# Kernel optimization log

Hardware: AMD Instinct MI355X
Metric: run time of the kernel (lower is better)

## Reference

```python
import jax, jax.numpy as jnp
import numpy as np

B, S, H, A, F = 16, 512, 768, 12, 3072
DH = H // A  # 64
EPS = 1e-5

def layernorm(x, w, b):
    mu = jnp.mean(x, axis=-1, keepdims=True)
    var = jnp.mean(jnp.square(x - mu), axis=-1, keepdims=True)
    return (x - mu) * jax.lax.rsqrt(var + EPS) * w + b

def setup_inputs() -> dict:
    key = jax.random.key(0)
    ks = jax.random.split(key, 12)
    std = 0.02
    inp = {
        "X": jax.random.normal(ks[0], (B, S, H), jnp.float32),
        "mask": jax.random.randint(ks[1], (B, S), 0, 2, jnp.int32),
        "WQ": jax.random.normal(ks[2], (H, H), jnp.float32) * std,
        "bQ": jnp.zeros((H,), jnp.float32),
        "WK": jax.random.normal(ks[3], (H, H), jnp.float32) * std,
        "bK": jnp.zeros((H,), jnp.float32),
        "WV": jax.random.normal(ks[4], (H, H), jnp.float32) * std,
        "bV": jnp.zeros((H,), jnp.float32),
        "WO": jax.random.normal(ks[5], (H, H), jnp.float32) * std,
        "bO": jnp.zeros((H,), jnp.float32),
        "ln1_w": jnp.ones((H,), jnp.float32),
        "ln1_b": jnp.zeros((H,), jnp.float32),
        "W1": jax.random.normal(ks[6], (H, F), jnp.float32) * std,
        "b1": jnp.zeros((F,), jnp.float32),
        "W2": jax.random.normal(ks[7], (F, H), jnp.float32) * std,
        "b2": jnp.zeros((H,), jnp.float32),
        "ln2_w": jnp.ones((H,), jnp.float32),
        "ln2_b": jnp.zeros((H,), jnp.float32),
    }
    return inp

def reference(X, mask, WQ, bQ, WK, bK, WV, bV, WO, bO, ln1_w, ln1_b, W1, b1, W2, b2, ln2_w, ln2_b):
    # --- multi-head self-attention (pretrained-weights branch, faithful reshapes) ---
    Q = (X @ WQ + bQ).reshape(B, A, S, DH)
    K = (X @ WK + bK).reshape(B, A, S, DH)
    V = (X @ WV + bV).reshape(B, A, S, DH)
    scores = jnp.einsum('bhqd,bhkd->bhqk', Q, K) / jnp.sqrt(jnp.float32(DH))
    scores = jnp.where(mask[:, None, None, :] == 0, -jnp.inf, scores)
    attn = jax.nn.softmax(scores, axis=-1)
    Z = jnp.einsum('bhqk,bhkd->bhqd', attn, V).reshape(B, S, H)
    attn_out = Z @ WO + bO
    # residual + LN (dropout is identity in eval)
    X = layernorm(attn_out + X, ln1_w, ln1_b)
    # --- FFN with exact GELU ---
    ffn = jax.nn.gelu(X @ W1 + b1, approximate=False) @ W2 + b2
    X = layernorm(ffn + X, ln2_w, ln2_b)
    return X
```

## Files before the change

kernel.cpp:

```cpp
#include <hip/hip_runtime.h>
#include <hip/hip_bf16.h>


using bf16_t = __hip_bfloat16;
typedef __bf16 bf16x8 __attribute__((ext_vector_type(8)));
typedef float f32x4 __attribute__((ext_vector_type(4)));

__device__ __forceinline__ float b2f(bf16_t v) { return __bfloat162float(v); }
__device__ __forceinline__ bf16_t f2b(float v) { return __float2bfloat16(v); }
__device__ __forceinline__ ushort f2bu(float v) { bf16_t b = f2b(v); return *(ushort*)&b; }

__device__ __forceinline__ void glds16(const ushort* g, ushort* l) {
    __builtin_amdgcn_global_load_lds(
        (const __attribute__((address_space(1))) unsigned int*)g,
        (__attribute__((address_space(3))) unsigned int*)l, 16, 0, 0);
}

__device__ __forceinline__ float gelu_f(float x) {
    float x2 = x * x;
    float y2 = 1.5957691216057308f * x * fmaf(0.044715f, x2, 1.0f);
    float e = __expf(y2);
    float t = 1.f - 2.f / (e + 1.f);
    return 0.5f * x * (1.f + t);
}

__device__ __forceinline__ void tr_tile(const float* __restrict__ in,
                                        bf16_t* __restrict__ out,
                                        int R, int C, int tx, int ty,
                                        float (*t)[65], int tid)
{
    int r0 = ty * 64, c0 = tx * 64;
    int tr = tid >> 6, tc = tid & 63;
#pragma unroll 4
    for (int i = 0; i < 16; ++i) {
        int r = i * 4 + tr;
        t[r][tc] = in[(size_t)(r0 + r) * C + c0 + tc];
    }
    __syncthreads();
#pragma unroll 4
    for (int i = 0; i < 16; ++i) {
        int r = i * 4 + tr;
        out[(size_t)(c0 + r) * R + r0 + tc] = f2b(t[tc][r]);
    }
}

__global__ __launch_bounds__(256) void prep_kernel(
    const float* __restrict__ WQ, const float* __restrict__ WK,
    const float* __restrict__ WV, const float* __restrict__ WO,
    const float* __restrict__ W1, const float* __restrict__ W2,
    const float* __restrict__ bQ, const float* __restrict__ bK,
    const float* __restrict__ bV, const float* __restrict__ X,
    bf16_t* __restrict__ Wqkv, bf16_t* __restrict__ WOt,
    bf16_t* __restrict__ W1t, bf16_t* __restrict__ W2t,
    float* __restrict__ bcat, bf16_t* __restrict__ Xb)
{
    __shared__ float t[64][65];
    const int blk = blockIdx.x, tid = threadIdx.x;
    if (blk < 576) {
        int m = blk / 144, tt = blk % 144;
        const float* in = (m == 0) ? WQ : (m == 1) ? WK : (m == 2) ? WV : WO;
        bf16_t* out = (m == 0) ? Wqkv : (m == 1) ? Wqkv + 589824
                    : (m == 2) ? Wqkv + 1179648 : WOt;
        tr_tile(in, out, 768, 768, tt % 12, tt / 12, t, tid);
    } else if (blk < 1152) {
        int tt = blk - 576;
        tr_tile(W1, W1t, 768, 3072, tt % 48, tt / 48, t, tid);
    } else if (blk < 1728) {
        int tt = blk - 1152;
        tr_tile(W2, W2t, 3072, 768, tt % 12, tt / 12, t, tid);
    } else if (blk == 1728) {
        for (int i = tid; i < 2304; i += 256)
            bcat[i] = (i < 768) ? bQ[i] : (i < 1536) ? bK[i - 768] : bV[i - 1536];
    } else {
        size_t i = ((size_t)(blk - 1729) * 256 + tid) * 8;
        float4 a = *(const float4*)(X + i);
        float4 b = *(const float4*)(X + i + 4);
#pragma unroll
        for (int j = 0; j < 4; ++j) {
            Xb[i + j]     = f2b(((const float*)&a)[j]);
            Xb[i + 4 + j] = f2b(((const float*)&b)[j]);
        }
    }
}

__global__ __launch_bounds__(256) void transpose_bf(
    const ushort* __restrict__ in, ushort* __restrict__ out,
    int R, int C, long inB, long outB)
{
    __shared__ ushort t[64][65];
    const ushort* ip = in + (size_t)blockIdx.z * inB;
    ushort* op = out + (size_t)blockIdx.z * outB;
    int r0 = blockIdx.y * 64, c0 = blockIdx.x * 64;
    int tr = threadIdx.x >> 6, tc = threadIdx.x & 63;
#pragma unroll 4
    for (int i = 0; i < 16; ++i) {
        int r = i * 4 + tr;
        t[r][tc] = ip[(size_t)(r0 + r) * C + c0 + tc];
    }
    __syncthreads();
#pragma unroll 4
    for (int i = 0; i < 16; ++i) {
        int r = i * 4 + tr;
        op[(size_t)(c0 + r) * R + r0 + tc] = t[tc][r];
    }
}

template <int EPI, int NTILE>
__global__ __launch_bounds__(256) void gemm128(
    const bf16_t* __restrict__ A, const bf16_t* __restrict__ Bt,
    const float* __restrict__ bias, const void* __restrict__ res,
    void* __restrict__ Cv, int K, int lda, int ldb, int ldc)
{
    __shared__ ushort lA[128 * 64];
    __shared__ ushort lB[NTILE * 64];
    constexpr int NI = NTILE / 32;
    const int tid = threadIdx.x;
    const int l = tid & 63, w = tid >> 6;
    const int l16 = l & 15, quad = l >> 4;
    const int m0 = blockIdx.x * 128, n0 = blockIdx.y * NTILE;

    const int srow = tid >> 3;
    const int sg = (((tid & 7) ^ (srow & 7)) << 3);
    const ushort* gA = (const ushort*)A + (size_t)(m0 + srow) * lda + sg;
    const ushort* gB = (const ushort*)Bt + (size_t)(n0 + srow) * ldb + sg;
    ushort* dA = lA + tid * 8;
    ushort* dB = lB + tid * 8;

    f32x4 acc[4][NI] = {};
    const int arow = (w & 1) * 64;
    const int brow = (w >> 1) * (NTILE / 2);

    for (int k0 = 0; k0 < K; k0 += 64) {
        __syncthreads();
        glds16(gA + k0,                      dA);
        glds16(gA + k0 + (size_t)32 * lda,   dA + 2048);
        glds16(gA + k0 + (size_t)64 * lda,   dA + 4096);
        glds16(gA + k0 + (size_t)96 * lda,   dA + 6144);
        glds16(gB + k0,                      dB);
        glds16(gB + k0 + (size_t)32 * ldb,   dB + 2048);
        if constexpr (NTILE == 128) {
            glds16(gB + k0 + (size_t)64 * ldb, dB + 4096);
            glds16(gB + k0 + (size_t)96 * ldb, dB + 6144);
        }
        __syncthreads();
#pragma unroll
        for (int kk = 0; kk < 2; ++kk) {
            const int pc = (((kk * 4 + quad) ^ (l16 & 7)) << 3);
            bf16x8 bfr[NI];
#pragma unroll
            for (int ni = 0; ni < NI; ++ni)
                bfr[ni] = *(const bf16x8*)&lB[(brow + ni * 16 + l16) * 64 + pc];
#pragma unroll
            for (int mi = 0; mi < 4; ++mi) {
                bf16x8 afr = *(const bf16x8*)&lA[(arow + mi * 16 + l16) * 64 + pc];
#pragma unroll
                for (int ni = 0; ni < NI; ++ni)
                    acc[mi][ni] = __builtin_amdgcn_mfma_f32_16x16x32_bf16(bfr[ni], afr, acc[mi][ni], 0, 0, 0);
            }
        }
    }

    float4 bv4[NI];
#pragma unroll
    for (int ni = 0; ni < NI; ++ni)
        bv4[ni] = *(const float4*)&bias[n0 + brow + ni * 16 + quad * 4];

#pragma unroll
    for (int mi = 0; mi < 4; ++mi) {
        int m = m0 + arow + mi * 16 + l16;
#pragma unroll
        for (int ni = 0; ni < NI; ++ni) {
            int nb = n0 + brow + ni * 16 + quad * 4;
            float v[4];
#pragma unroll
            for (int r = 0; r < 4; ++r) v[r] = acc[mi][ni][r] + ((const float*)&bv4[ni])[r];
            if constexpr (EPI == 1) {
#pragma unroll
                for (int r = 0; r < 4; ++r) v[r] = gelu_f(v[r]);
            } else if constexpr (EPI == 2) {
                float4 r4 = *(const float4*)&((const float*)res)[(size_t)m * ldc + nb];
#pragma unroll
                for (int r = 0; r < 4; ++r) v[r] += ((const float*)&r4)[r];
            } else if constexpr (EPI == 5) {
                ushort4 rb = *(const ushort4*)&((const ushort*)res)[(size_t)m * ldc + nb];
#pragma unroll
                for (int r = 0; r < 4; ++r) v[r] += b2f(*(const bf16_t*)&((const ushort*)&rb)[r]);
            }
            if constexpr (EPI == 5) {
                *(float4*)&((float*)Cv)[(size_t)m * ldc + nb] = make_float4(v[0], v[1], v[2], v[3]);
            } else {
                ushort4 st;
                st.x = f2bu(v[0]); st.y = f2bu(v[1]); st.z = f2bu(v[2]); st.w = f2bu(v[3]);
                if constexpr (EPI == 6) {
                    bf16_t* Cseg = (bf16_t*)Cv + (size_t)(n0 / 768) * 6291456;
                    int nloc = (n0 % 768) + brow + ni * 16 + quad * 4;
                    *(ushort4*)&((ushort*)Cseg)[(size_t)m * 768 + nloc] = st;
                } else {
                    *(ushort4*)&((ushort*)Cv)[(size_t)m * ldc + nb] = st;
                }
            }
        }
    }
}

__global__ __launch_bounds__(256) void flash_kernel(
    const bf16_t* __restrict__ Q, const bf16_t* __restrict__ Kx,
    const bf16_t* __restrict__ Vt, const int* __restrict__ mask,
    bf16_t* __restrict__ Z)
{
    __shared__ ushort lK[64 * 64];
    __shared__ ushort lV[64 * 64];
    __shared__ ushort lP[64 * 72];

    const int h = blockIdx.y;
    const int q0 = blockIdx.x * 64;
    const ushort* Qh = (const ushort*)Q + (size_t)h * 32768;
    const ushort* Kh = (const ushort*)Kx + (size_t)h * 32768;
    const ushort* Vh = (const ushort*)Vt + (size_t)h * 32768;
    const int* mk = mask + (h / 12) * 512;
    ushort* Zh = (ushort*)Z + (size_t)h * 32768;

    const int tid = threadIdx.x;
    const int l = tid & 63, w = tid >> 6;
    const int l16 = l & 15, quad = l >> 4;

    bf16x8 qfr[2];
#pragma unroll
    for (int kk = 0; kk < 2; ++kk)
        qfr[kk] = *(const bf16x8*)(Qh + (size_t)(q0 + w * 16 + l16) * 64 + kk * 32 + quad * 8);

    const int c8p = tid & 7;
    const int kr0 = tid >> 3;
    float m_i = -1e30f, l_i = 0.f;
    f32x4 o4[4] = {};

    for (int kt = 0; kt < 8; ++kt) {
#pragma unroll
        for (int p = 0; p < 2; ++p) {
            int row = kr0 + p * 32;
            int c8l = c8p ^ (row & 7);
            glds16(Kh + (size_t)(kt * 64 + row) * 64 + c8l * 8, lK + (p * 256 + tid) * 8);
            glds16(Vh + (size_t)row * 512 + kt * 64 + c8l * 8, lV + (p * 256 + tid) * 8);
        }
        __syncthreads();

        f32x4 s4[4] = {};
#pragma unroll
        for (int kk = 0; kk < 2; ++kk) {
#pragma unroll
            for (int nt = 0; nt < 4; ++nt) {
                bf16x8 kfr = *(const bf16x8*)&lK[(nt * 16 + l16) * 64 + (((kk * 4 + quad) ^ (l16 & 7)) << 3)];
                s4[nt] = __builtin_amdgcn_mfma_f32_16x16x32_bf16(kfr, qfr[kk], s4[nt], 0, 0, 0);
            }
        }

        float pv[4][4];
        float rm = -1e30f;
#pragma unroll
        for (int nt = 0; nt < 4; ++nt) {
            int4 m4 = *(const int4*)&mk[kt * 64 + nt * 16 + quad * 4];
#pragma unroll
            for (int r = 0; r < 4; ++r) {
                float v = (((const int*)&m4)[r] == 0) ? -1e30f : s4[nt][r] * 0.125f;
                pv[nt][r] = v;
                rm = fmaxf(rm, v);
            }
        }
        rm = fmaxf(rm, __shfl_xor(rm, 16));
        rm = fmaxf(rm, __shfl_xor(rm, 32));
        float mn = fmaxf(m_i, rm);
        float al = __expf(m_i - mn);
        float rs = 0.f;
#pragma unroll
        for (int nt = 0; nt < 4; ++nt)
#pragma unroll
            for (int r = 0; r < 4; ++r) {
                float e = __expf(pv[nt][r] - mn);
                pv[nt][r] = e;
                rs += e;
            }
        rs += __shfl_xor(rs, 16);
        rs += __shfl_xor(rs, 32);
        l_i = l_i * al + rs;
        m_i = mn;
#pragma unroll
        for (int dt = 0; dt < 4; ++dt)
#pragma unroll
            for (int r = 0; r < 4; ++r) o4[dt][r] *= al;

#pragma unroll
        for (int nt = 0; nt < 4; ++nt) {
            ushort4 st;
            st.x = f2bu(pv[nt][0]); st.y = f2bu(pv[nt][1]);
            st.z = f2bu(pv[nt][2]); st.w = f2bu(pv[nt][3]);
            *(ushort4*)&lP[(w * 16 + l16) * 72 + nt * 16 + quad * 4] = st;
        }
        __syncthreads();

#pragma unroll
        for (int kk = 0; kk < 2; ++kk) {
            bf16x8 pafr = *(const bf16x8*)&lP[(w * 16 + l16) * 72 + kk * 32 + quad * 8];
#pragma unroll
            for (int dt = 0; dt < 4; ++dt) {
                bf16x8 bvfr = *(const bf16x8*)&lV[(dt * 16 + l16) * 64 + (((kk * 4 + quad) ^ (l16 & 7)) << 3)];
                o4[dt] = __builtin_amdgcn_mfma_f32_16x16x32_bf16(bvfr, pafr, o4[dt], 0, 0, 0);
            }
        }
        __syncthreads();
    }

    float inv = 1.f / l_i;
#pragma unroll
    for (int dt = 0; dt < 4; ++dt) {
        ushort4 st;
        st.x = f2bu(o4[dt][0] * inv); st.y = f2bu(o4[dt][1] * inv);
        st.z = f2bu(o4[dt][2] * inv); st.w = f2bu(o4[dt][3] * inv);
        *(ushort4*)&Zh[(size_t)(q0 + w * 16 + l16) * 64 + dt * 16 + quad * 4] = st;
    }
}

__device__ __forceinline__ float to_f(float v)  { return v; }
__device__ __forceinline__ float to_f(bf16_t v) { return b2f(v); }
__device__ __forceinline__ void from_f(float& d, float v)  { d = v; }
__device__ __forceinline__ void from_f(bf16_t& d, float v) { d = f2b(v); }

template <typename TI, typename TO>
__global__ __launch_bounds__(256) void layernorm_kernel(
    const TI* __restrict__ X, const float* __restrict__ w,
    const float* __restrict__ b, TO* __restrict__ out)
{
    const TI* x = X + (size_t)blockIdx.x * 768;
    TO* o = out + (size_t)blockIdx.x * 768;
    int t = threadIdx.x;
    float v[3];
    float s = 0.f, sq = 0.f;
#pragma unroll
    for (int i = 0; i < 3; ++i) {
        v[i] = to_f(x[t + i * 256]);
        s += v[i]; sq += v[i] * v[i];
    }
#pragma unroll
    for (int off = 32; off; off >>= 1) { s += __shfl_xor(s, off); sq += __shfl_xor(sq, off); }
    __shared__ float s1[4], s2[4];
    int wave = t >> 6, lane = t & 63;
    if (lane == 0) { s1[wave] = s; s2[wave] = sq; }
    __syncthreads();
    s  = s1[0] + s1[1] + s1[2] + s1[3];
    sq = s2[0] + s2[1] + s2[2] + s2[3];
    float mu  = s * (1.f / 768.f);
    float var = sq * (1.f / 768.f) - mu * mu;
    float rs  = rsqrtf(var + 1e-5f);
#pragma unroll
    for (int i = 0; i < 3; ++i)
        from_f(o[t + i * 256], (v[i] - mu) * rs * w[t + i * 256] + b[t + i * 256]);
}

extern "C" void kernel_launch(void* const* d_in, const int* in_sizes, int n_in,
                              void* d_out, int out_size, void* d_ws, size_t ws_size,
                              hipStream_t stream)
{
    const float* X    = (const float*)d_in[0];
    const int*   mask = (const int*)  d_in[1];
    const float* WQ   = (const float*)d_in[2];
    const float* bQ   = (const float*)d_in[3];
    const float* WK   = (const float*)d_in[4];
    const float* bK   = (const float*)d_in[5];
    const float* WV   = (const float*)d_in[6];
    const float* bV   = (const float*)d_in[7];
    const float* WO   = (const float*)d_in[8];
    const float* bO   = (const float*)d_in[9];
    const float* ln1w = (const float*)d_in[10];
    const float* ln1b = (const float*)d_in[11];
    const float* W1   = (const float*)d_in[12];
    const float* b1   = (const float*)d_in[13];
    const float* W2   = (const float*)d_in[14];
    const float* b2   = (const float*)d_in[15];
    const float* ln2w = (const float*)d_in[16];
    const float* ln2b = (const float*)d_in[17];
    float* out = (float*)d_out;

    bf16_t* ws   = (bf16_t*)d_ws;
    bf16_t* Wqkv = ws;
    bf16_t* WOt  = Wqkv + 1769472;
    bf16_t* W1t  = WOt + 589824;
    bf16_t* W2t  = W1t + 2359296;
    float*  bcat = (float*)(W2t + 2359296);
    bf16_t* Qb   = W2t + 2359296 + 4608;
    bf16_t* Kb   = Qb + 6291456;
    bf16_t* Vb   = Kb + 6291456;
    bf16_t* Xb   = Vb + 6291456;
    bf16_t* Vt   = Xb + 6291456;
    bf16_t* Zb = Qb;
    bf16_t* Y1 = Xb;
    bf16_t* X1 = Qb;
    bf16_t* Hb = Kb;

    prep_kernel<<<4801, 256, 0, stream>>>(WQ, WK, WV, WO, W1, W2, bQ, bK, bV, X,
                                          Wqkv, WOt, W1t, W2t, bcat, Xb);

    gemm128<6, 128><<<dim3(64, 18), 256, 0, stream>>>(Xb, Wqkv, bcat, nullptr, Qb,
                                                      768, 768, 768, 768);

    transpose_bf<<<dim3(1, 8, 192), 256, 0, stream>>>((const ushort*)Vb, (ushort*)Vt,
                                                      512, 64, 32768, 32768);

    flash_kernel<<<dim3(8, 192), 256, 0, stream>>>(Qb, Kb, Vt, mask, Zb);

    gemm128<2, 64><<<dim3(64, 12), 256, 0, stream>>>(Zb, WOt, bO, X, Y1,
                                                     768, 768, 768, 768);
    layernorm_kernel<bf16_t, bf16_t><<<8192, 256, 0, stream>>>(Y1, ln1w, ln1b, X1);

    gemm128<1, 128><<<dim3(64, 24), 256, 0, stream>>>(X1, W1t, b1, nullptr, Hb,
                                                      768, 768, 768, 3072);
    gemm128<5, 64><<<dim3(64, 12), 256, 0, stream>>>(Hb, W2t, b2, X1, out,
                                                     3072, 3072, 3072, 768);
    layernorm_kernel<float, float><<<8192, 256, 0, stream>>>(out, ln2w, ln2b, out);
}
```

Baseline: 379.7 us.

## Fuse V transpose into QKV GEMM epilogue and double flash query tile

The QKV GEMM epilogue now writes the V segment straight into the per-head transposed layout, which removes the separate transpose kernel launch and one round trip of V through memory. The flash attention kernel now handles 128 query rows per block, two 16-row MFMA subtiles per wave, so each K/V tile loaded into LDS is reused twice as much. The cost is scattered 2-byte strided stores in the GEMM epilogue, more registers and LDS in the flash kernel, and half as many flash blocks.

```diff
diff --git a/kernel.cpp b/kernel.cpp
--- a/kernel.cpp
+++ b/kernel.cpp
@@ -83,28 +83,6 @@
     }
 }
 
-__global__ __launch_bounds__(256) void transpose_bf(
-    const ushort* __restrict__ in, ushort* __restrict__ out,
-    int R, int C, long inB, long outB)
-{
-    __shared__ ushort t[64][65];
-    const ushort* ip = in + (size_t)blockIdx.z * inB;
-    ushort* op = out + (size_t)blockIdx.z * outB;
-    int r0 = blockIdx.y * 64, c0 = blockIdx.x * 64;
-    int tr = threadIdx.x >> 6, tc = threadIdx.x & 63;
-#pragma unroll 4
-    for (int i = 0; i < 16; ++i) {
-        int r = i * 4 + tr;
-        t[r][tc] = ip[(size_t)(r0 + r) * C + c0 + tc];
-    }
-    __syncthreads();
-#pragma unroll 4
-    for (int i = 0; i < 16; ++i) {
-        int r = i * 4 + tr;
-        op[(size_t)(c0 + r) * R + r0 + tc] = t[tc][r];
-    }
-}
-
 template <int EPI, int NTILE>
 __global__ __launch_bounds__(256) void gemm128(
     const bf16_t* __restrict__ A, const bf16_t* __restrict__ Bt,
@@ -192,9 +170,24 @@
                 ushort4 st;
                 st.x = f2bu(v[0]); st.y = f2bu(v[1]); st.z = f2bu(v[2]); st.w = f2bu(v[3]);
                 if constexpr (EPI == 6) {
-                    bf16_t* Cseg = (bf16_t*)Cv + (size_t)(n0 / 768) * 6291456;
-                    int nloc = (n0 % 768) + brow + ni * 16 + quad * 4;
-                    *(ushort4*)&((ushort*)Cseg)[(size_t)m * 768 + nloc] = st;
+                    int seg = n0 / 768;
+                    if (seg < 2) {
+                        bf16_t* Cseg = (bf16_t*)Cv + (size_t)seg * 6291456;
+                        int nloc = (n0 % 768) + brow + ni * 16 + quad * 4;
+                        *(ushort4*)&((ushort*)Cseg)[(size_t)m * 768 + nloc] = st;
+                    } else {
+                        ushort* vt = (ushort*)res;
+                        int nloc = (n0 - 1536) + brow + ni * 16 + quad * 4;
+                        int fb = (m & 511) * 768 + nloc;
+                        int h = (m >> 9) * 12 + (fb >> 15);
+                        int d = fb & 63;
+                        int s = (fb >> 6) & 511;
+                        ushort* vh = vt + (size_t)h * 32768 + s;
+                        vh[(size_t)(d + 0) * 512] = st.x;
+                        vh[(size_t)(d + 1) * 512] = st.y;
+                        vh[(size_t)(d + 2) * 512] = st.z;
+                        vh[(size_t)(d + 3) * 512] = st.w;
+                    }
                 } else {
                     *(ushort4*)&((ushort*)Cv)[(size_t)m * ldc + nb] = st;
                 }
@@ -210,10 +203,10 @@
 {
     __shared__ ushort lK[64 * 64];
     __shared__ ushort lV[64 * 64];
-    __shared__ ushort lP[64 * 72];
+    __shared__ ushort lP[128 * 72];
 
     const int h = blockIdx.y;
-    const int q0 = blockIdx.x * 64;
+    const int q0 = blockIdx.x * 128;
     const ushort* Qh = (const ushort*)Q + (size_t)h * 32768;
     const ushort* Kh = (const ushort*)Kx + (size_t)h * 32768;
     const ushort* Vh = (const ushort*)Vt + (size_t)h * 32768;
@@ -224,15 +217,17 @@
     const int l = tid & 63, w = tid >> 6;
     const int l16 = l & 15, quad = l >> 4;
 
-    bf16x8 qfr[2];
-#pragma unroll
-    for (int kk = 0; kk < 2; ++kk)
-        qfr[kk] = *(const bf16x8*)(Qh + (size_t)(q0 + w * 16 + l16) * 64 + kk * 32 + quad * 8);
+    bf16x8 qfr[2][2];
+#pragma unroll
+    for (int mi = 0; mi < 2; ++mi)
+#pragma unroll
+        for (int kk = 0; kk < 2; ++kk)
+            qfr[mi][kk] = *(const bf16x8*)(Qh + (size_t)(q0 + w * 32 + mi * 16 + l16) * 64 + kk * 32 + quad * 8);
 
     const int c8p = tid & 7;
     const int kr0 = tid >> 3;
-    float m_i = -1e30f, l_i = 0.f;
-    f32x4 o4[4] = {};
+    float m_i[2] = {-1e30f, -1e30f}, l_i[2] = {0.f, 0.f};
+    f32x4 o4[2][4] = {};
 
     for (int kt = 0; kt < 8; ++kt) {
 #pragma unroll
@@ -244,78 +239,91 @@
         }
         __syncthreads();
 
-        f32x4 s4[4] = {};
+        f32x4 s4[2][4] = {};
 #pragma unroll
         for (int kk = 0; kk < 2; ++kk) {
 #pragma unroll
             for (int nt = 0; nt < 4; ++nt) {
                 bf16x8 kfr = *(const bf16x8*)&lK[(nt * 16 + l16) * 64 + (((kk * 4 + quad) ^ (l16 & 7)) << 3)];
-                s4[nt] = __builtin_amdgcn_mfma_f32_16x16x32_bf16(kfr, qfr[kk], s4[nt], 0, 0, 0);
-            }
-        }
-
-        float pv[4][4];
-        float rm = -1e30f;
-#pragma unroll
-        for (int nt = 0; nt < 4; ++nt) {
-            int4 m4 = *(const int4*)&mk[kt * 64 + nt * 16 + quad * 4];
-#pragma unroll
-            for (int r = 0; r < 4; ++r) {
-                float v = (((const int*)&m4)[r] == 0) ? -1e30f : s4[nt][r] * 0.125f;
-                pv[nt][r] = v;
-                rm = fmaxf(rm, v);
-            }
-        }
-        rm = fmaxf(rm, __shfl_xor(rm, 16));
-        rm = fmaxf(rm, __shfl_xor(rm, 32));
-        float mn = fmaxf(m_i, rm);
-        float al = __expf(m_i - mn);
-        float rs = 0.f;
-#pragma unroll
-        for (int nt = 0; nt < 4; ++nt)
-#pragma unroll
-            for (int r = 0; r < 4; ++r) {
-                float e = __expf(pv[nt][r] - mn);
-                pv[nt][r] = e;
-                rs += e;
-            }
-        rs += __shfl_xor(rs, 16);
-        rs += __shfl_xor(rs, 32);
-        l_i = l_i * al + rs;
-        m_i = mn;
-#pragma unroll
-        for (int dt = 0; dt < 4; ++dt)
-#pragma unroll
-            for (int r = 0; r < 4; ++r) o4[dt][r] *= al;
-
-#pragma unroll
-        for (int nt = 0; nt < 4; ++nt) {
-            ushort4 st;
-            st.x = f2bu(pv[nt][0]); st.y = f2bu(pv[nt][1]);
-            st.z = f2bu(pv[nt][2]); st.w = f2bu(pv[nt][3]);
-            *(ushort4*)&lP[(w * 16 + l16) * 72 + nt * 16 + quad * 4] = st;
+#pragma unroll
+                for (int mi = 0; mi < 2; ++mi)
+                    s4[mi][nt] = __builtin_amdgcn_mfma_f32_16x16x32_bf16(kfr, qfr[mi][kk], s4[mi][nt], 0, 0, 0);
+            }
+        }
+
+        int4 m4[4];
+#pragma unroll
+        for (int nt = 0; nt < 4; ++nt) m4[nt] = *(const int4*)&mk[kt * 64 + nt * 16 + quad * 4];
+
+#pragma unroll
+        for (int mi = 0; mi < 2; ++mi) {
+            float pv[4][4];
+            float rm = -1e30f;
+#pragma unroll
+            for (int nt = 0; nt < 4; ++nt)
+#pragma unroll
+                for (int r = 0; r < 4; ++r) {
+                    float v = (((const int*)&m4[nt])[r] == 0) ? -1e30f : s4[mi][nt][r] * 0.125f;
+                    pv[nt][r] = v;
+                    rm = fmaxf(rm, v);
+                }
+            rm = fmaxf(rm, __shfl_xor(rm, 16));
+            rm = fmaxf(rm, __shfl_xor(rm, 32));
+            float mn = fmaxf(m_i[mi], rm);
+            float al = __expf(m_i[mi] - mn);
+            float rs = 0.f;
+#pragma unroll
+            for (int nt = 0; nt < 4; ++nt)
+#pragma unroll
+                for (int r = 0; r < 4; ++r) {
+                    float e = __expf(pv[nt][r] - mn);
+                    pv[nt][r] = e;
+                    rs += e;
+                }
+            rs += __shfl_xor(rs, 16);
+            rs += __shfl_xor(rs, 32);
+            l_i[mi] = l_i[mi] * al + rs;
+            m_i[mi] = mn;
+#pragma unroll
+            for (int dt = 0; dt < 4; ++dt)
+#pragma unroll
+                for (int r = 0; r < 4; ++r) o4[mi][dt][r] *= al;
+
+#pragma unroll
+            for (int nt = 0; nt < 4; ++nt) {
+                ushort4 st;
+                st.x = f2bu(pv[nt][0]); st.y = f2bu(pv[nt][1]);
+                st.z = f2bu(pv[nt][2]); st.w = f2bu(pv[nt][3]);
+                *(ushort4*)&lP[(w * 32 + mi * 16 + l16) * 72 + nt * 16 + quad * 4] = st;
+            }
         }
         __syncthreads();
 
 #pragma unroll
         for (int kk = 0; kk < 2; ++kk) {
-            bf16x8 pafr = *(const bf16x8*)&lP[(w * 16 + l16) * 72 + kk * 32 + quad * 8];
 #pragma unroll
             for (int dt = 0; dt < 4; ++dt) {
                 bf16x8 bvfr = *(const bf16x8*)&lV[(dt * 16 + l16) * 64 + (((kk * 4 + quad) ^ (l16 & 7)) << 3)];
-                o4[dt] = __builtin_amdgcn_mfma_f32_16x16x32_bf16(bvfr, pafr, o4[dt], 0, 0, 0);
+#pragma unroll
+                for (int mi = 0; mi < 2; ++mi) {
+                    bf16x8 pafr = *(const bf16x8*)&lP[(w * 32 + mi * 16 + l16) * 72 + kk * 32 + quad * 8];
+                    o4[mi][dt] = __builtin_amdgcn_mfma_f32_16x16x32_bf16(bvfr, pafr, o4[mi][dt], 0, 0, 0);
+                }
             }
         }
         __syncthreads();
     }
 
-    float inv = 1.f / l_i;
-#pragma unroll
-    for (int dt = 0; dt < 4; ++dt) {
-        ushort4 st;
-        st.x = f2bu(o4[dt][0] * inv); st.y = f2bu(o4[dt][1] * inv);
-        st.z = f2bu(o4[dt][2] * inv); st.w = f2bu(o4[dt][3] * inv);
-        *(ushort4*)&Zh[(size_t)(q0 + w * 16 + l16) * 64 + dt * 16 + quad * 4] = st;
+#pragma unroll
+    for (int mi = 0; mi < 2; ++mi) {
+        float inv = 1.f / l_i[mi];
+#pragma unroll
+        for (int dt = 0; dt < 4; ++dt) {
+            ushort4 st;
+            st.x = f2bu(o4[mi][dt][0] * inv); st.y = f2bu(o4[mi][dt][1] * inv);
+            st.z = f2bu(o4[mi][dt][2] * inv); st.w = f2bu(o4[mi][dt][3] * inv);
+            *(ushort4*)&Zh[(size_t)(q0 + w * 32 + mi * 16 + l16) * 64 + dt * 16 + quad * 4] = st;
+        }
     }
 }
 
@@ -398,13 +406,10 @@
     prep_kernel<<<4801, 256, 0, stream>>>(WQ, WK, WV, WO, W1, W2, bQ, bK, bV, X,
                                           Wqkv, WOt, W1t, W2t, bcat, Xb);
 
-    gemm128<6, 128><<<dim3(64, 18), 256, 0, stream>>>(Xb, Wqkv, bcat, nullptr, Qb,
+    gemm128<6, 128><<<dim3(64, 18), 256, 0, stream>>>(Xb, Wqkv, bcat, Vt, Qb,
                                                       768, 768, 768, 768);
 
-    transpose_bf<<<dim3(1, 8, 192), 256, 0, stream>>>((const ushort*)Vb, (ushort*)Vt,
-                                                      512, 64, 32768, 32768);
-
-    flash_kernel<<<dim3(8, 192), 256, 0, stream>>>(Qb, Kb, Vt, mask, Zb);
+    flash_kernel<<<dim3(4, 192), 256, 0, stream>>>(Qb, Kb, Vt, mask, Zb);
 
     gemm128<2, 64><<<dim3(64, 12), 256, 0, stream>>>(Zb, WOt, bO, X, Y1,
                                                      768, 768, 768, 768);
```

Result: no change. 379.7 us (+0.0%).
